# Optimization experiments

Measured on AMD Instinct MI355X. Metric: run time of the kernel, lower is better.

Reference implementation:

```python
import jax, jax.numpy as jnp
import numpy as np
import math

D_MODEL = 1024
N_HEADS = 16
HEAD_DIM = D_MODEL // N_HEADS
BAND_RADIUS = 2
BAND_VAL = 0.1


def setup_inputs() -> dict:
    key = jax.random.key(0)
    ks = jax.random.split(key, 12)
    B, S = 4, 2048
    scale = 1.0 / math.sqrt(D_MODEL)
    inp = {
        "x": jax.random.normal(ks[0], (B, S, D_MODEL), dtype=jnp.float32),
        "ocr_context": jax.random.normal(ks[1], (B, S, D_MODEL), dtype=jnp.float32),
        "Wq": jax.random.normal(ks[2], (D_MODEL, D_MODEL), dtype=jnp.float32) * scale,
        "bq": jnp.zeros((D_MODEL,), dtype=jnp.float32),
        "Wk": jax.random.normal(ks[3], (D_MODEL, D_MODEL), dtype=jnp.float32) * scale,
        "bk": jnp.zeros((D_MODEL,), dtype=jnp.float32),
        "Wv": jax.random.normal(ks[4], (D_MODEL, D_MODEL), dtype=jnp.float32) * scale,
        "bv": jnp.zeros((D_MODEL,), dtype=jnp.float32),
        "Wo": jax.random.normal(ks[5], (D_MODEL, D_MODEL), dtype=jnp.float32) * scale,
        "bo": jnp.zeros((D_MODEL,), dtype=jnp.float32),
        "ocr_bias": jax.random.normal(ks[6], (D_MODEL,), dtype=jnp.float32),
    }
    return inp


def _band_mask(S, dtype):
    # additive mask: 0.1 inside |i-j| <= 2, else 0 (matches _create_ocr_pattern_mask)
    i = jnp.arange(S)
    band = (jnp.abs(i[:, None] - i[None, :]) <= BAND_RADIUS).astype(dtype) * BAND_VAL
    return band[None, None, :, :]  # [1,1,S,S], broadcasts over batch & heads


def reference(x, ocr_context, Wq, bq, Wk, bk, Wv, bv, Wo, bo, ocr_bias):
    B, S, _ = x.shape
    # torch Linear: x @ W.T + b
    q = x @ Wq.T + bq + ocr_bias  # ocr bias added to q before head split
    k = x @ Wk.T + bk
    v = x @ Wv.T + bv
    q = q.reshape(B, S, N_HEADS, HEAD_DIM).transpose(0, 2, 1, 3)  # [B,H,S,d]
    k = k.reshape(B, S, N_HEADS, HEAD_DIM).transpose(0, 2, 1, 3)
    v = v.reshape(B, S, N_HEADS, HEAD_DIM).transpose(0, 2, 1, 3)
    scores = jnp.einsum("bhsd,bhtd->bhst", q, k) / math.sqrt(HEAD_DIM)
    scores = scores + _band_mask(S, scores.dtype)  # ocr_context only supplies shape
    attn = jax.nn.softmax(scores, axis=-1)
    out = jnp.einsum("bhst,bhtd->bhsd", attn, v)
    out = out.transpose(0, 2, 1, 3).reshape(B, S, D_MODEL)
    return out @ Wo.T + bo
```

## Files before the change

### kernel.cpp

```cpp
#include <hip/hip_runtime.h>
#include <hip/hip_bf16.h>
#include <stdint.h>

typedef __attribute__((ext_vector_type(8))) short bf16x8;
typedef __attribute__((ext_vector_type(4))) float f32x4;
typedef __attribute__((ext_vector_type(16))) float f32x16;
typedef __attribute__((ext_vector_type(4))) unsigned u32x4;

#define L2E 1.4426950408889634f

static __device__ __forceinline__ unsigned short f2bf(float f) {
    __hip_bfloat16 h = __float2bfloat16(f);
    return __builtin_bit_cast(unsigned short, h);
}

static __device__ __forceinline__ void gl2lds16(const void* g, void* l) {
    __builtin_amdgcn_global_load_lds(
        (const __attribute__((address_space(1))) void*)g,
        (__attribute__((address_space(3))) void*)l,
        16, 0, 0);
}

__global__ void cast_kernel(const float* __restrict__ src,
                            unsigned short* __restrict__ dst, int n4) {
    int i = blockIdx.x * blockDim.x + threadIdx.x;
    int stride = gridDim.x * blockDim.x;
    for (; i < n4; i += stride) {
        float4 v = ((const float4*)src)[i];
        ushort4 o;
        o.x = f2bf(v.x); o.y = f2bf(v.y); o.z = f2bf(v.z); o.w = f2bf(v.w);
        ((ushort4*)dst)[i] = o;
    }
}

template<int OM>
__global__ __launch_bounds__(256) void gemm_bt(
    const unsigned short* __restrict__ A,
    const unsigned short* __restrict__ W,
    const float* __restrict__ bias,
    const float* __restrict__ bias2,
    float scale,
    unsigned short* __restrict__ obf,
    float* __restrict__ of)
{
    constexpr int K = 1024;
    __shared__ unsigned short As[128][64];
    __shared__ unsigned short Bs[128][64];

    const int tid  = threadIdx.x;
    const int wave = tid >> 6, lane = tid & 63;
    const int li = lane & 15, lg = lane >> 4;
    const int lin = blockIdx.y * 8 + blockIdx.x;
    const int n2  = (lin & 7) * 64 + (lin >> 3);
    const int m0 = (n2 >> 3) * 128, n0 = (n2 & 7) * 128;
    const int wm = (wave >> 1) * 64, wn = (wave & 1) * 64;

    const int srow = wave * 8 + (lane >> 3);
    const int scol = (lane & 7) * 8;

    f32x4 acc[4][4] = {};

    for (int k0 = 0; k0 < K; k0 += 64) {
#pragma unroll
        for (int rnd = 0; rnd < 4; ++rnd)
            gl2lds16(A + (size_t)(m0 + rnd * 32 + srow) * K + k0 + scol,
                     &As[rnd * 32 + wave * 8][0]);
#pragma unroll
        for (int rnd = 0; rnd < 4; ++rnd)
            gl2lds16(W + (size_t)(n0 + rnd * 32 + srow) * K + k0 + scol,
                     &Bs[rnd * 32 + wave * 8][0]);
        __syncthreads();
#pragma unroll
        for (int kk = 0; kk < 64; kk += 32) {
            bf16x8 af[4], bfr[4];
#pragma unroll
            for (int m = 0; m < 4; ++m)
                af[m] = *(const bf16x8*)&As[wm + m * 16 + li][kk + lg * 8];
#pragma unroll
            for (int n = 0; n < 4; ++n)
                bfr[n] = *(const bf16x8*)&Bs[wn + n * 16 + li][kk + lg * 8];
#pragma unroll
            for (int m = 0; m < 4; ++m)
#pragma unroll
                for (int n = 0; n < 4; ++n)
                    acc[m][n] = __builtin_amdgcn_mfma_f32_16x16x32_bf16(
                        af[m], bfr[n], acc[m][n], 0, 0, 0);
        }
        __syncthreads();
    }

#pragma unroll
    for (int n = 0; n < 4; ++n) {
        const int col = n0 + wn + n * 16 + li;
        float bb = bias[col];
        if (bias2) bb += bias2[col];
#pragma unroll
        for (int m = 0; m < 4; ++m) {
            if (OM == 2) {
                const int row0 = m0 + wm + m * 16 + lg * 4;
                size_t addr = ((size_t)(((row0 >> 11) << 4) + (col >> 6)) * 64 + (col & 63)) * 2048
                              + (row0 & 2047);
                ushort4 o;
                o.x = f2bf((acc[m][n][0] + bb) * scale);
                o.y = f2bf((acc[m][n][1] + bb) * scale);
                o.z = f2bf((acc[m][n][2] + bb) * scale);
                o.w = f2bf((acc[m][n][3] + bb) * scale);
                *(ushort4*)&obf[addr] = o;
            } else {
#pragma unroll
                for (int r = 0; r < 4; ++r) {
                    const int row = m0 + wm + m * 16 + lg * 4 + r;
                    float v = (acc[m][n][r] + bb) * scale;
                    if (OM == 1) of[(size_t)row * 1024 + col] = v;
                    else         obf[(size_t)row * 1024 + col] = f2bf(v);
                }
            }
        }
    }
}

__global__ __launch_bounds__(256, 4) void attn_kernel(
    const unsigned short* __restrict__ Q,
    const unsigned short* __restrict__ Km,
    const unsigned short* __restrict__ VT,
    unsigned short* __restrict__ AO)
{
    __shared__ unsigned short Ks[2][4096];
    __shared__ unsigned short Vs[2][4096];

    const int tid  = threadIdx.x;
    const int w = tid >> 6, lane = tid & 63;
    const int li5 = lane & 31, l5 = lane >> 5, li7 = li5 & 7;

    const int p  = blockIdx.y * 16 + blockIdx.x;
    const int q_ = (p & 7) * 128 + (p >> 3);
    const int bx = q_ & 15, bh = q_ >> 4;
    const int b = bh >> 4, h = bh & 15;
    const int qb = bx * 128 + w * 32;
    const int qrow = qb + li5;

    const int srow = w * 16 + (lane >> 3);
    const int swz  = ((lane & 7) ^ (lane >> 3)) * 8;

    const unsigned short* Kg0 = Km + (size_t)(b * 2048 + srow) * 1024 + h * 64 + swz;
    const unsigned short* Vg0 = VT + ((size_t)bh * 64 + srow) * 2048 + swz;

    bf16x8 qf[4];
#pragma unroll
    for (int f = 0; f < 4; ++f)
        qf[f] = *(const bf16x8*)&Q[(size_t)(b * 2048 + qrow) * 1024 + h * 64
                                   + f * 16 + l5 * 8];

    f32x16 acc[2] = {};
    float lr = 0.f;

#pragma unroll
    for (int it = 0; it < 2; ++it) {
        gl2lds16(Kg0 + (size_t)(it * 8) * 1024, &Ks[0][(w * 2 + it) * 512]);
        gl2lds16(Vg0 + (size_t)(it * 8) * 2048, &Vs[0][(w * 2 + it) * 512]);
    }
    __syncthreads();

    for (int t = 0; t < 32; ++t) {
        const int buf = t & 1;
        const int j0 = t * 64;
        if (t < 31) {
            const int j1 = j0 + 64;
#pragma unroll
            for (int it = 0; it < 2; ++it) {
                gl2lds16(Kg0 + (size_t)(j1 + it * 8) * 1024, &Ks[buf ^ 1][(w * 2 + it) * 512]);
                gl2lds16(Vg0 + (size_t)(it * 8) * 2048 + j1, &Vs[buf ^ 1][(w * 2 + it) * 512]);
            }
        }

        f32x16 st[2];
        __builtin_amdgcn_s_setprio(1);
#pragma unroll
        for (int jf = 0; jf < 2; ++jf) {
            f32x16 z = {};
#pragma unroll
            for (int f = 0; f < 4; ++f) {
                bf16x8 kf = *(const bf16x8*)&Ks[buf][(jf * 32 + li5) * 64
                                                     + ((f * 2 + l5) ^ li7) * 8];
                z = __builtin_amdgcn_mfma_f32_32x32x16_bf16(kf, qf[f], z, 0, 0, 0);
            }
            st[jf] = z;
        }
        __builtin_amdgcn_s_setprio(0);

        if (j0 >= qb - 65 && j0 <= qb + 33) {
#pragma unroll
            for (int jf = 0; jf < 2; ++jf)
#pragma unroll
                for (int r = 0; r < 16; ++r) {
                    int j = j0 + jf * 32 + (r & 3) + 8 * (r >> 2) + 4 * l5;
                    int dq = qrow - j;
                    if ((unsigned)(dq + 2) <= 4u) st[jf][r] += 0.1f * L2E;
                }
        }

        unsigned pw[2][8];
        float ps = 0.f;
#pragma unroll
        for (int jf = 0; jf < 2; ++jf)
#pragma unroll
            for (int m = 0; m < 8; ++m) {
                float p0 = __builtin_amdgcn_exp2f(st[jf][2 * m]);
                float p1 = __builtin_amdgcn_exp2f(st[jf][2 * m + 1]);
                ps += p0 + p1;
                pw[jf][m] = (unsigned)f2bf(p0) | ((unsigned)f2bf(p1) << 16);
            }
        lr += ps;

#pragma unroll
        for (int jf = 0; jf < 2; ++jf)
#pragma unroll
            for (int m2 = 0; m2 < 2; ++m2)
#pragma unroll
                for (int m0_ = 0; m0_ < 2; ++m0_) {
                    unsigned a0 = pw[jf][m2 * 4 + m0_];
                    unsigned b0 = pw[jf][m2 * 4 + m0_ + 2];
                    asm volatile("v_permlane32_swap_b32 %0, %1"
                                 : "+v"(a0), "+v"(b0));
                    pw[jf][m2 * 4 + m0_]     = a0;
                    pw[jf][m2 * 4 + m0_ + 2] = b0;
                }

        __builtin_amdgcn_s_setprio(1);
#pragma unroll
        for (int db = 0; db < 2; ++db)
#pragma unroll
            for (int tt = 0; tt < 4; ++tt) {
                bf16x8 vf = *(const bf16x8*)&Vs[buf][(db * 32 + li5) * 64
                                                     + ((tt * 2 + l5) ^ li7) * 8];
                const int jf = tt >> 1, m2 = tt & 1;
                u32x4 tw = {pw[jf][m2 * 4 + 0], pw[jf][m2 * 4 + 1],
                            pw[jf][m2 * 4 + 2], pw[jf][m2 * 4 + 3]};
                acc[db] = __builtin_amdgcn_mfma_f32_32x32x16_bf16(
                    vf, __builtin_bit_cast(bf16x8, tw), acc[db], 0, 0, 0);
            }
        __builtin_amdgcn_s_setprio(0);
        __syncthreads();
    }

    float l2 = lr + __shfl_xor(lr, 32);
    const float inv = 1.f / l2;
#pragma unroll
    for (int db = 0; db < 2; ++db)
#pragma unroll
        for (int g = 0; g < 4; ++g) {
            ushort4 o;
            o.x = f2bf(acc[db][g * 4 + 0] * inv);
            o.y = f2bf(acc[db][g * 4 + 1] * inv);
            o.z = f2bf(acc[db][g * 4 + 2] * inv);
            o.w = f2bf(acc[db][g * 4 + 3] * inv);
            *(ushort4*)&AO[(size_t)(b * 2048 + qrow) * 1024 + h * 64
                           + db * 32 + g * 8 + l5 * 4] = o;
        }
}

extern "C" void kernel_launch(void* const* d_in, const int* in_sizes, int n_in,
                              void* d_out, int out_size, void* d_ws, size_t ws_size,
                              hipStream_t stream) {
    const float* x   = (const float*)d_in[0];
    const float* Wq  = (const float*)d_in[2];
    const float* bq  = (const float*)d_in[3];
    const float* Wk  = (const float*)d_in[4];
    const float* bk  = (const float*)d_in[5];
    const float* Wv  = (const float*)d_in[6];
    const float* bv  = (const float*)d_in[7];
    const float* Wo  = (const float*)d_in[8];
    const float* bo  = (const float*)d_in[9];
    const float* ocr = (const float*)d_in[10];
    float* out = (float*)d_out;

    char* ws = (char*)d_ws;
    const size_t MB = 1024 * 1024;
    unsigned short* xb  = (unsigned short*)(ws);
    unsigned short* Wqb = (unsigned short*)(ws + 16 * MB);
    unsigned short* Wkb = (unsigned short*)(ws + 18 * MB);
    unsigned short* Wvb = (unsigned short*)(ws + 20 * MB);
    unsigned short* Wob = (unsigned short*)(ws + 22 * MB);
    unsigned short* Qb  = (unsigned short*)(ws + 24 * MB);
    unsigned short* Kb  = (unsigned short*)(ws + 40 * MB);
    unsigned short* VTb = (unsigned short*)(ws + 56 * MB);
    unsigned short* AO  = xb;

    cast_kernel<<<2048, 256, 0, stream>>>(x,  xb,  8388608 / 4);
    cast_kernel<<<512,  256, 0, stream>>>(Wq, Wqb, 1048576 / 4);
    cast_kernel<<<512,  256, 0, stream>>>(Wk, Wkb, 1048576 / 4);
    cast_kernel<<<512,  256, 0, stream>>>(Wv, Wvb, 1048576 / 4);
    cast_kernel<<<512,  256, 0, stream>>>(Wo, Wob, 1048576 / 4);

    dim3 g(8, 64);
    const float QSC = 0.125f * L2E;
    gemm_bt<0><<<g, 256, 0, stream>>>(xb, Wqb, bq, ocr,     QSC, Qb,  nullptr);
    gemm_bt<0><<<g, 256, 0, stream>>>(xb, Wkb, bk, nullptr, 1.f, Kb,  nullptr);
    gemm_bt<2><<<g, 256, 0, stream>>>(xb, Wvb, bv, nullptr, 1.f, VTb, nullptr);

    attn_kernel<<<dim3(16, 64), 256, 0, stream>>>(Qb, Kb, VTb, AO);

    gemm_bt<1><<<g, 256, 0, stream>>>(AO, Wob, bo, nullptr, 1.f, nullptr, out);
}
```

Measured before the change: 229.8 us.

## Fuse QKV projections into one GEMM launch and batch weight casts

Merges the three Q/K/V projection GEMMs into a single launch with a 24x64 grid, where each block picks its weight, bias and output layout at run time. The four weight cast kernels become one 2D-grid kernel. In the attention kernel, the softmax row sum is split across four accumulators and the bf16 packing uses v_cvt_pk_bf16_f32. The aim is to cut launch overhead and tail effects and to shorten the exp/pack dependency chain, at the cost of runtime branching on projection type inside the GEMM.

Result: faster. 197.6 us (-14.0%).

```diff
diff --git a/kernel.cpp b/kernel.cpp
--- a/kernel.cpp
+++ b/kernel.cpp
@@ -33,14 +33,122 @@
     }
 }
 
-template<int OM>
-__global__ __launch_bounds__(256) void gemm_bt(
+__global__ void cast4_kernel(const float* __restrict__ s0, const float* __restrict__ s1,
+                             const float* __restrict__ s2, const float* __restrict__ s3,
+                             unsigned short* __restrict__ d0, unsigned short* __restrict__ d1,
+                             unsigned short* __restrict__ d2, unsigned short* __restrict__ d3) {
+    const int m = blockIdx.y;
+    const float* src = m == 0 ? s0 : m == 1 ? s1 : m == 2 ? s2 : s3;
+    unsigned short* dst = m == 0 ? d0 : m == 1 ? d1 : m == 2 ? d2 : d3;
+    int i = blockIdx.x * blockDim.x + threadIdx.x;
+    for (; i < 262144; i += 256 * 256) {
+        float4 v = ((const float4*)src)[i];
+        ushort4 o;
+        o.x = f2bf(v.x); o.y = f2bf(v.y); o.z = f2bf(v.z); o.w = f2bf(v.w);
+        ((ushort4*)dst)[i] = o;
+    }
+}
+
+__global__ __launch_bounds__(256) void qkv_gemm(
+    const unsigned short* __restrict__ A,
+    const unsigned short* __restrict__ Wq,
+    const unsigned short* __restrict__ Wk,
+    const unsigned short* __restrict__ Wv,
+    const float* __restrict__ bq,
+    const float* __restrict__ bk,
+    const float* __restrict__ bv,
+    const float* __restrict__ ocr,
+    float qscale,
+    unsigned short* __restrict__ Qo,
+    unsigned short* __restrict__ Ko,
+    unsigned short* __restrict__ VTo)
+{
+    constexpr int K = 1024;
+    __shared__ unsigned short As[128][64];
+    __shared__ unsigned short Bs[128][64];
+
+    const int tid  = threadIdx.x;
+    const int wave = tid >> 6, lane = tid & 63;
+    const int li = lane & 15, lg = lane >> 4;
+
+    const int lin = blockIdx.y * 24 + blockIdx.x;
+    const int n2  = (lin & 7) * 192 + (lin >> 3);
+    const int mb = n2 / 24, nbb = n2 - mb * 24;
+    const int proj = nbb >> 3;
+    const int m0 = mb * 128, n0 = (nbb & 7) * 128;
+
+    const unsigned short* W = proj == 0 ? Wq : proj == 1 ? Wk : Wv;
+    const float* bias = proj == 0 ? bq : proj == 1 ? bk : bv;
+
+    const int wm = (wave >> 1) * 64, wn = (wave & 1) * 64;
+    const int srow = wave * 8 + (lane >> 3);
+    const int scol = (lane & 7) * 8;
+
+    f32x4 acc[4][4] = {};
+
+    for (int k0 = 0; k0 < K; k0 += 64) {
+#pragma unroll
+        for (int rnd = 0; rnd < 4; ++rnd)
+            gl2lds16(A + (size_t)(m0 + rnd * 32 + srow) * K + k0 + scol,
+                     &As[rnd * 32 + wave * 8][0]);
+#pragma unroll
+        for (int rnd = 0; rnd < 4; ++rnd)
+            gl2lds16(W + (size_t)(n0 + rnd * 32 + srow) * K + k0 + scol,
+                     &Bs[rnd * 32 + wave * 8][0]);
+        __syncthreads();
+#pragma unroll
+        for (int kk = 0; kk < 64; kk += 32) {
+            bf16x8 af[4], bfr[4];
+#pragma unroll
+            for (int m = 0; m < 4; ++m)
+                af[m] = *(const bf16x8*)&As[wm + m * 16 + li][kk + lg * 8];
+#pragma unroll
+            for (int n = 0; n < 4; ++n)
+                bfr[n] = *(const bf16x8*)&Bs[wn + n * 16 + li][kk + lg * 8];
+#pragma unroll
+            for (int m = 0; m < 4; ++m)
+#pragma unroll
+                for (int n = 0; n < 4; ++n)
+                    acc[m][n] = __builtin_amdgcn_mfma_f32_16x16x32_bf16(
+                        af[m], bfr[n], acc[m][n], 0, 0, 0);
+        }
+        __syncthreads();
+    }
+
+    const float scale = proj == 0 ? qscale : 1.f;
+#pragma unroll
+    for (int n = 0; n < 4; ++n) {
+        const int col = n0 + wn + n * 16 + li;
+        float bb = bias[col];
+        if (proj == 0) bb += ocr[col];
+#pragma unroll
+        for (int m = 0; m < 4; ++m) {
+            if (proj == 2) {
+                const int row0 = m0 + wm + m * 16 + lg * 4;
+                size_t addr = ((size_t)(((row0 >> 11) << 4) + (col >> 6)) * 64 + (col & 63)) * 2048
+                              + (row0 & 2047);
+                ushort4 o;
+                o.x = f2bf(acc[m][n][0] + bb);
+                o.y = f2bf(acc[m][n][1] + bb);
+                o.z = f2bf(acc[m][n][2] + bb);
+                o.w = f2bf(acc[m][n][3] + bb);
+                *(ushort4*)&VTo[addr] = o;
+            } else {
+                unsigned short* dst = proj == 0 ? Qo : Ko;
+#pragma unroll
+                for (int r = 0; r < 4; ++r) {
+                    const int row = m0 + wm + m * 16 + lg * 4 + r;
+                    dst[(size_t)row * 1024 + col] = f2bf((acc[m][n][r] + bb) * scale);
+                }
+            }
+        }
+    }
+}
+
+__global__ __launch_bounds__(256) void out_gemm(
     const unsigned short* __restrict__ A,
     const unsigned short* __restrict__ W,
     const float* __restrict__ bias,
-    const float* __restrict__ bias2,
-    float scale,
-    unsigned short* __restrict__ obf,
     float* __restrict__ of)
 {
     constexpr int K = 1024;
@@ -92,30 +200,14 @@
 #pragma unroll
     for (int n = 0; n < 4; ++n) {
         const int col = n0 + wn + n * 16 + li;
-        float bb = bias[col];
-        if (bias2) bb += bias2[col];
-#pragma unroll
-        for (int m = 0; m < 4; ++m) {
-            if (OM == 2) {
-                const int row0 = m0 + wm + m * 16 + lg * 4;
-                size_t addr = ((size_t)(((row0 >> 11) << 4) + (col >> 6)) * 64 + (col & 63)) * 2048
-                              + (row0 & 2047);
-                ushort4 o;
-                o.x = f2bf((acc[m][n][0] + bb) * scale);
-                o.y = f2bf((acc[m][n][1] + bb) * scale);
-                o.z = f2bf((acc[m][n][2] + bb) * scale);
-                o.w = f2bf((acc[m][n][3] + bb) * scale);
-                *(ushort4*)&obf[addr] = o;
-            } else {
-#pragma unroll
-                for (int r = 0; r < 4; ++r) {
-                    const int row = m0 + wm + m * 16 + lg * 4 + r;
-                    float v = (acc[m][n][r] + bb) * scale;
-                    if (OM == 1) of[(size_t)row * 1024 + col] = v;
-                    else         obf[(size_t)row * 1024 + col] = f2bf(v);
-                }
-            }
-        }
+        const float bb = bias[col];
+#pragma unroll
+        for (int m = 0; m < 4; ++m)
+#pragma unroll
+            for (int r = 0; r < 4; ++r) {
+                const int row = m0 + wm + m * 16 + lg * 4 + r;
+                of[(size_t)row * 1024 + col] = acc[m][n][r] + bb;
+            }
     }
 }
 
@@ -152,7 +244,7 @@
                                    + f * 16 + l5 * 8];
 
     f32x16 acc[2] = {};
-    float lr = 0.f;
+    float ls0 = 0.f, ls1 = 0.f, ls2 = 0.f, ls3 = 0.f;
 
 #pragma unroll
     for (int it = 0; it < 2; ++it) {
@@ -200,17 +292,24 @@
         }
 
         unsigned pw[2][8];
-        float ps = 0.f;
-#pragma unroll
-        for (int jf = 0; jf < 2; ++jf)
+#pragma unroll
+        for (int jf = 0; jf < 2; ++jf) {
 #pragma unroll
             for (int m = 0; m < 8; ++m) {
                 float p0 = __builtin_amdgcn_exp2f(st[jf][2 * m]);
                 float p1 = __builtin_amdgcn_exp2f(st[jf][2 * m + 1]);
-                ps += p0 + p1;
-                pw[jf][m] = (unsigned)f2bf(p0) | ((unsigned)f2bf(p1) << 16);
-            }
-        lr += ps;
+                if (m == 0) { ls0 += p0; ls1 += p1; }
+                else if (m == 1) { ls2 += p0; ls3 += p1; }
+                else if (m == 2) { ls0 += p0; ls1 += p1; }
+                else if (m == 3) { ls2 += p0; ls3 += p1; }
+                else if (m == 4) { ls0 += p0; ls1 += p1; }
+                else if (m == 5) { ls2 += p0; ls3 += p1; }
+                else if (m == 6) { ls0 += p0; ls1 += p1; }
+                else             { ls2 += p0; ls3 += p1; }
+                asm("v_cvt_pk_bf16_f32 %0, %1, %2"
+                    : "=v"(pw[jf][m]) : "v"(p0), "v"(p1));
+            }
+        }
 
 #pragma unroll
         for (int jf = 0; jf < 2; ++jf)
@@ -243,6 +342,7 @@
         __syncthreads();
     }
 
+    float lr = (ls0 + ls1) + (ls2 + ls3);
     float l2 = lr + __shfl_xor(lr, 32);
     const float inv = 1.f / l2;
 #pragma unroll
@@ -286,19 +386,16 @@
     unsigned short* VTb = (unsigned short*)(ws + 56 * MB);
     unsigned short* AO  = xb;
 
-    cast_kernel<<<2048, 256, 0, stream>>>(x,  xb,  8388608 / 4);
-    cast_kernel<<<512,  256, 0, stream>>>(Wq, Wqb, 1048576 / 4);
-    cast_kernel<<<512,  256, 0, stream>>>(Wk, Wkb, 1048576 / 4);
-    cast_kernel<<<512,  256, 0, stream>>>(Wv, Wvb, 1048576 / 4);
-    cast_kernel<<<512,  256, 0, stream>>>(Wo, Wob, 1048576 / 4);
-
-    dim3 g(8, 64);
+    cast_kernel<<<2048, 256, 0, stream>>>(x, xb, 8388608 / 4);
+    cast4_kernel<<<dim3(256, 4), 256, 0, stream>>>(Wq, Wk, Wv, Wo,
+                                                   Wqb, Wkb, Wvb, Wob);
+
     const float QSC = 0.125f * L2E;
-    gemm_bt<0><<<g, 256, 0, stream>>>(xb, Wqb, bq, ocr,     QSC, Qb,  nullptr);
-    gemm_bt<0><<<g, 256, 0, stream>>>(xb, Wkb, bk, nullptr, 1.f, Kb,  nullptr);
-    gemm_bt<2><<<g, 256, 0, stream>>>(xb, Wvb, bv, nullptr, 1.f, VTb, nullptr);
+    qkv_gemm<<<dim3(24, 64), 256, 0, stream>>>(xb, Wqb, Wkb, Wvb,
+                                               bq, bk, bv, ocr, QSC,
+                                               Qb, Kb, VTb);
 
     attn_kernel<<<dim3(16, 64), 256, 0, stream>>>(Qb, Kb, VTb, AO);
 
-    gemm_bt<1><<<g, 256, 0, stream>>>(AO, Wob, bo, nullptr, 1.f, nullptr, out);
-}
+    out_gemm<<<dim3(8, 64), 256, 0, stream>>>(AO, Wob, bo, out);
+}
```
